# Performance work log

Hardware: AMD Instinct MI355X
Metric: run time of the kernel (lower is better)

Reference implementation:

```python
import jax, jax.numpy as jnp
import numpy as np

N_TOTAL = 200000
DIM = 256
N_GRAPHS = 8192
N_ITERS = 6


def setup_inputs() -> dict:
    key = jax.random.key(0)
    k1, k2, k3, k4, k5, k6 = jax.random.split(key, 6)
    x = jax.random.normal(k1, (N_TOTAL, DIM), dtype=jnp.float32)
    batch = jnp.sort(jax.random.randint(k2, (N_TOTAL,), 0, N_GRAPHS)).astype(jnp.int32)
    bound = 1.0 / np.sqrt(DIM)
    W_ih = jax.random.uniform(k3, (4 * DIM, DIM), jnp.float32, -bound, bound)
    W_hh = jax.random.uniform(k4, (4 * DIM, DIM), jnp.float32, -bound, bound)
    b_ih = jax.random.uniform(k5, (4 * DIM,), jnp.float32, -bound, bound)
    b_hh = jax.random.uniform(k6, (4 * DIM,), jnp.float32, -bound, bound)
    return {"x": x, "batch": batch, "n_graphs": N_GRAPHS,
            "W_ih": W_ih, "W_hh": W_hh, "b_ih": b_ih, "b_hh": b_hh}


def _lstm_cell(inp, h, c, W_ih, W_hh, b_ih, b_hh):
    # PyTorch LSTMCell: gates ordered i, f, g, o
    gates = inp @ W_ih.T + b_ih + h @ W_hh.T + b_hh
    i, f, g, o = jnp.split(gates, 4, axis=-1)
    c_new = jax.nn.sigmoid(f) * c + jax.nn.sigmoid(i) * jnp.tanh(g)
    h_new = jax.nn.sigmoid(o) * jnp.tanh(c_new)
    return h_new, c_new


def reference(x, batch, n_graphs, W_ih, W_hh, b_ih, b_hh):
    dim = x.shape[1]
    h = jnp.zeros((n_graphs, dim), x.dtype)
    c = jnp.zeros((n_graphs, dim), x.dtype)
    readout = jnp.zeros((n_graphs, dim), x.dtype)
    for _ in range(N_ITERS):
        # attention scores per node: <x_v, q_{g(v)}>
        scores = jnp.sum(x * h[batch], axis=-1)  # (N,)
        # torch scatter_reduce_ amax with zero init includes the 0 -> max(seg_max, 0)
        seg_max = jax.ops.segment_max(scores, batch, num_segments=n_graphs,
                                      indices_are_sorted=True)
        seg_max = jnp.maximum(seg_max, 0.0)
        e = jnp.exp(scores - seg_max[batch])
        seg_sum = jax.ops.segment_sum(e, batch, num_segments=n_graphs,
                                      indices_are_sorted=True)
        w = e / (seg_sum[batch] + 1e-8)  # (N,)
        readout = jax.ops.segment_sum(x * w[:, None], batch, num_segments=n_graphs,
                                      indices_are_sorted=True)  # (G, dim)
        h, c = _lstm_cell(readout, h, c, W_ih, W_hh, b_ih, b_hh)
    return jnp.concatenate([h, readout], axis=-1)  # (G, 2*dim)
```

## Files before the change

### kernel.cpp

```cpp
#include <hip/hip_runtime.h>
#include <hip/hip_bf16.h>
#include <hip/hip_fp16.h>
#include <stdint.h>

#define DIM 256
#define NG 8192
#define KDIM 512
#define GDIM 1024
#define N_ITERS 6

#define BM 128
#define BN 128
#define BK 64

typedef __hip_bfloat16 bf16;
typedef __attribute__((ext_vector_type(8))) short bf16x8;
typedef __attribute__((ext_vector_type(4))) float f32x4;
typedef __attribute__((ext_vector_type(8))) unsigned short u16x8;
typedef __attribute__((ext_vector_type(4))) unsigned short u16x4;

__device__ __forceinline__ void async16(void* lds, const void* g) {
    __builtin_amdgcn_global_load_lds((const __attribute__((address_space(1))) void*)g,
                                     (__attribute__((address_space(3))) void*)lds, 16, 0, 0);
}
__device__ __forceinline__ float fast_sigmoid(float v) {
    return 1.0f / (1.0f + __expf(-v));
}
__device__ __forceinline__ float fast_tanh(float v) {
    float e = __expf(2.0f * v);
    return (e - 1.0f) / (e + 1.0f);
}
__device__ __forceinline__ unsigned short f2bf(float v) {
    __hip_bfloat16 t = __float2bfloat16(v);
    unsigned short u; __builtin_memcpy(&u, &t, 2); return u;
}
__device__ __forceinline__ unsigned short f2h(float v) {
    __half t = __float2half_rn(v);
    unsigned short u; __builtin_memcpy(&u, &t, 2); return u;
}
__device__ __forceinline__ float h2f(unsigned short u) {
    __half t; __builtin_memcpy(&t, &u, 2);
    return __half2float(t);
}

__global__ void k_prep(const int* __restrict__ batch, int n_nodes, int* __restrict__ offs,
                       const float* __restrict__ Wih, const float* __restrict__ Whh,
                       const float* __restrict__ bih, const float* __restrict__ bhh,
                       bf16* __restrict__ Wcat, float* __restrict__ bsum,
                       float* __restrict__ h, float* __restrict__ c, bf16* __restrict__ Acat0) {
    const int idx = blockIdx.x * blockDim.x + threadIdx.x;
    if (idx < NG * DIM) {
        h[idx] = 0.0f; c[idx] = 0.0f;
        Acat0[(size_t)(idx >> 8) * KDIM + DIM + (idx & 255)] = __float2bfloat16(0.0f);
    }
    if (idx < GDIM * KDIM) {
        const int n = idx >> 9;
        const int k = idx & (KDIM - 1);
        const int d = n >> 2, gate = n & 3;
        const int j = gate * DIM + d;
        const float v = (k < DIM) ? Wih[j * DIM + k] : Whh[j * DIM + (k - DIM)];
        Wcat[idx] = __float2bfloat16(v);
    }
    if (idx < GDIM) {
        const int d = idx >> 2, gate = idx & 3;
        const int j = gate * DIM + d;
        bsum[idx] = bih[j] + bhh[j];
    }
    if (idx < n_nodes) {
        const int b = batch[idx];
        const int bp = (idx == 0) ? -1 : batch[idx - 1];
        for (int g = bp + 1; g <= b; ++g) offs[g] = idx;
        if (idx == n_nodes - 1)
            for (int g = b + 1; g <= NG; ++g) offs[g] = n_nodes;
    }
}

template <bool FIRST, bool LAST>
__global__ __launch_bounds__(256) void k_att(const float* __restrict__ xf,
                                             unsigned short* __restrict__ xb,
                                             const float* __restrict__ h,
                                             const int* __restrict__ offs,
                                             float* __restrict__ rout,
                                             bf16* __restrict__ AcatOut) {
    const int wave = threadIdx.x >> 6;
    const int g = (blockIdx.x << 2) + wave;
    const int lane = threadIdx.x & 63;
    const int half = lane >> 5, hl = lane & 31;

    float hreg[8];
    {
        const float4 a = *(const float4*)&h[(size_t)g * DIM + hl * 8];
        const float4 b = *(const float4*)&h[(size_t)g * DIM + hl * 8 + 4];
        hreg[0] = a.x; hreg[1] = a.y; hreg[2] = a.z; hreg[3] = a.w;
        hreg[4] = b.x; hreg[5] = b.y; hreg[6] = b.z; hreg[7] = b.w;
    }

    const int start = offs[g], end = offs[g + 1];
    float racc[8] = {0, 0, 0, 0, 0, 0, 0, 0};
    float m = 0.0f;
    float s = 0.0f;

    for (int r0 = start; r0 < end; r0 += 2) {
        const int r = r0 + half;
        const bool valid = (r < end);
        float xv[8];
        float dt = 0.0f;
        if (valid) {
            if (FIRST) {
                const float4 a = *(const float4*)&xf[(size_t)r * DIM + hl * 8];
                const float4 b = *(const float4*)&xf[(size_t)r * DIM + hl * 8 + 4];
                xv[0] = a.x; xv[1] = a.y; xv[2] = a.z; xv[3] = a.w;
                xv[4] = b.x; xv[5] = b.y; xv[6] = b.z; xv[7] = b.w;
                u16x8 pk;
                #pragma unroll
                for (int j = 0; j < 8; ++j) pk[j] = f2h(xv[j]);
                *(u16x8*)&xb[(size_t)r * DIM + hl * 8] = pk;
            } else {
                const u16x8 pk = *(const u16x8*)&xb[(size_t)r * DIM + hl * 8];
                #pragma unroll
                for (int j = 0; j < 8; ++j) xv[j] = h2f(pk[j]);
            }
            #pragma unroll
            for (int j = 0; j < 8; ++j) dt = fmaf(xv[j], hreg[j], dt);
        }
        #pragma unroll
        for (int off = 16; off > 0; off >>= 1) dt += __shfl_xor(dt, off);
        if (valid) {
            const float mn = fmaxf(m, dt);
            const float al = __expf(m - mn);
            const float e  = __expf(dt - mn);
            s = s * al + e;
            #pragma unroll
            for (int j = 0; j < 8; ++j) racc[j] = fmaf(racc[j], al, e * xv[j]);
            m = mn;
        }
    }

    const float mo = __shfl_xor(m, 32);
    const float M  = fmaxf(m, mo);
    const float al = __expf(m - M);
    s *= al;
    #pragma unroll
    for (int j = 0; j < 8; ++j) racc[j] *= al;
    s += __shfl_xor(s, 32);
    #pragma unroll
    for (int j = 0; j < 8; ++j) racc[j] += __shfl_xor(racc[j], 32);
    const float inv = 1.0f / (s + 1e-8f);
    float o[8];
    #pragma unroll
    for (int j = 0; j < 8; ++j) o[j] = racc[j] * inv;

    if (half == 0) {
        u16x8 pk;
        #pragma unroll
        for (int j = 0; j < 8; ++j) pk[j] = f2bf(o[j]);
        *(u16x8*)&AcatOut[(size_t)g * KDIM + hl * 8] = pk;
    } else if (LAST) {
        *(float4*)&rout[(size_t)g * KDIM + hl * 8]     = make_float4(o[0], o[1], o[2], o[3]);
        *(float4*)&rout[(size_t)g * KDIM + hl * 8 + 4] = make_float4(o[4], o[5], o[6], o[7]);
    }
}

template <bool LAST>
__global__ __launch_bounds__(256) void k_gemm_cell(const bf16* __restrict__ A,
                                                   const bf16* __restrict__ W,
                                                   const float* __restrict__ bsum,
                                                   float* __restrict__ cst,
                                                   float* __restrict__ hst,
                                                   bf16* __restrict__ AcatN,
                                                   float* __restrict__ hout) {
    __shared__ union {
        struct { bf16 As[BM * BK]; bf16 Bs[BN * BK]; } st;
        float ep[32][132];
    } sm;

    const int tid = threadIdx.x;
    const int wave = tid >> 6, lane = tid & 63;
    const int m0 = blockIdx.x * BM;
    const int n0 = blockIdx.y * BN;
    const int wr = wave >> 1, wc = wave & 1;

    f32x4 acc[4][4] = {};
    const int chunk = lane & 7;

    for (int k0 = 0; k0 < KDIM; k0 += BK) {
        #pragma unroll
        for (int i = 0; i < 4; ++i) {
            const int grp = wave * 32 + i * 8;
            async16(&sm.st.As[grp * BK],
                    A + (size_t)(m0 + grp + (lane >> 3)) * KDIM + k0 + chunk * 8);
        }
        #pragma unroll
        for (int i = 0; i < 4; ++i) {
            const int grp = wave * 32 + i * 8;
            async16(&sm.st.Bs[grp * BK],
                    W + (size_t)(n0 + grp + (lane >> 3)) * KDIM + k0 + chunk * 8);
        }
        asm volatile("s_waitcnt vmcnt(0)" ::: "memory");
        __syncthreads();

        #pragma unroll
        for (int ks = 0; ks < BK; ks += 32) {
            bf16x8 a[4], b[4];
            #pragma unroll
            for (int mi = 0; mi < 4; ++mi)
                a[mi] = *(const bf16x8*)&sm.st.As[(wr * 64 + mi * 16 + (lane & 15)) * BK + ks + (lane >> 4) * 8];
            #pragma unroll
            for (int ni = 0; ni < 4; ++ni)
                b[ni] = *(const bf16x8*)&sm.st.Bs[(wc * 64 + ni * 16 + (lane & 15)) * BK + ks + (lane >> 4) * 8];
            #pragma unroll
            for (int mi = 0; mi < 4; ++mi)
                #pragma unroll
                for (int ni = 0; ni < 4; ++ni)
                    acc[mi][ni] = __builtin_amdgcn_mfma_f32_16x16x32_bf16(a[mi], b[ni], acc[mi][ni], 0, 0, 0);
        }
        __syncthreads();
    }

    float bv[4];
    #pragma unroll
    for (int ni = 0; ni < 4; ++ni)
        bv[ni] = bsum[n0 + wc * 64 + ni * 16 + (lane & 15)];

    const int d0 = n0 >> 2;
    const int lr = tid >> 3;
    const int dd = (tid & 7) * 4;

    #pragma unroll
    for (int mi = 0; mi < 4; ++mi) {
        __syncthreads();
        #pragma unroll
        for (int ni = 0; ni < 4; ++ni) {
            const int colL = wc * 64 + ni * 16 + (lane & 15);
            #pragma unroll
            for (int r = 0; r < 4; ++r) {
                const int lrow = wr * 16 + (lane >> 4) * 4 + r;
                sm.ep[lrow][colL] = acc[mi][ni][r] + bv[ni];
            }
        }
        __syncthreads();
        const int grow = m0 + (lr >> 4) * 64 + mi * 16 + (lr & 15);
        const int d = d0 + dd;
        float co[4], cn[4], hn[4];
        *(float4*)co = *(const float4*)&cst[(size_t)grow * DIM + d];
        u16x4 hb;
        #pragma unroll
        for (int j = 0; j < 4; ++j) {
            const float4 q = *(const float4*)&sm.ep[lr][(dd + j) * 4];
            cn[j] = fast_sigmoid(q.y) * co[j] + fast_sigmoid(q.x) * fast_tanh(q.z);
            hn[j] = fast_sigmoid(q.w) * fast_tanh(cn[j]);
            hb[j] = f2bf(hn[j]);
        }
        if (LAST) {
            *(float4*)&hout[(size_t)grow * KDIM + d] = *(float4*)hn;
        } else {
            *(float4*)&cst[(size_t)grow * DIM + d] = *(float4*)cn;
            *(float4*)&hst[(size_t)grow * DIM + d] = *(float4*)hn;
            *(u16x4*)&AcatN[(size_t)grow * KDIM + DIM + d] = hb;
        }
    }
}

extern "C" void kernel_launch(void* const* d_in, const int* in_sizes, int n_in,
                              void* d_out, int out_size, void* d_ws, size_t ws_size,
                              hipStream_t stream) {
    const float* x     = (const float*)d_in[0];
    const int*   batch = (const int*)d_in[1];
    const float* Wih   = (const float*)d_in[3];
    const float* Whh   = (const float*)d_in[4];
    const float* bih   = (const float*)d_in[5];
    const float* bhh   = (const float*)d_in[6];
    const int n_nodes  = in_sizes[0] / DIM;
    float* out = (float*)d_out;

    char* ws = (char*)d_ws;
    size_t off = 0;
    auto alloc = [&](size_t bytes) -> void* {
        off = (off + 255) & ~(size_t)255;
        void* p = ws + off;
        off += bytes;
        return p;
    };
    int*   offs  = (int*)  alloc((size_t)(NG + 1) * sizeof(int));
    bf16*  Wcat  = (bf16*) alloc((size_t)GDIM * KDIM * sizeof(bf16));
    float* bsum  = (float*)alloc((size_t)GDIM * sizeof(float));
    bf16*  Acat0 = (bf16*) alloc((size_t)NG * KDIM * sizeof(bf16));
    bf16*  Acat1 = (bf16*) alloc((size_t)NG * KDIM * sizeof(bf16));
    float* h     = (float*)alloc((size_t)NG * DIM * sizeof(float));
    float* c     = (float*)alloc((size_t)NG * DIM * sizeof(float));
    unsigned short* xb = (unsigned short*)alloc((size_t)n_nodes * DIM * sizeof(unsigned short));
    (void)ws_size; (void)n_in; (void)out_size;

    k_prep<<<NG * DIM / 256, 256, 0, stream>>>(batch, n_nodes, offs, Wih, Whh, bih, bhh,
                                               Wcat, bsum, h, c, Acat0);

    for (int it = 0; it < N_ITERS; ++it) {
        bf16* Ain  = (it & 1) ? Acat1 : Acat0;
        bf16* Aout = (it & 1) ? Acat0 : Acat1;
        if (it == 0)
            k_att<true, false><<<NG / 4, 256, 0, stream>>>(x, xb, h, offs, nullptr, Ain);
        else if (it < N_ITERS - 1)
            k_att<false, false><<<NG / 4, 256, 0, stream>>>(x, xb, h, offs, nullptr, Ain);
        else
            k_att<false, true><<<NG / 4, 256, 0, stream>>>(x, xb, h, offs, out + DIM, Ain);

        if (it < N_ITERS - 1)
            k_gemm_cell<false><<<dim3(NG / BM, GDIM / BN), 256, 0, stream>>>(
                Ain, Wcat, bsum, c, h, Aout, nullptr);
        else
            k_gemm_cell<true><<<dim3(NG / BM, GDIM / BN), 256, 0, stream>>>(
                Ain, Wcat, bsum, c, nullptr, nullptr, out);
    }
}
```

Measured before the change: 832.5 us.

## Fuse all phases into one persistent cooperative kernel with grid syncs

Replaces the 13 separate launches (prep, attention and GEMM+cell per iteration) with a single cooperative kernel of 512 blocks that separates phases with grid.sync. Each wave now handles four graphs in the attention phase, and the next row's x load is software-prefetched while the current one is processed. The aim is to remove launch gaps and tail effects between phases. The cost is fewer resident waves for the memory-bound attention phase, grid-wide barrier overhead, and a launch-bounds occupancy constraint of two blocks per CU that may limit GEMM registers. A fallback path with normal launches runs if the cooperative launch fails.

```diff
diff --git a/kernel.cpp b/kernel.cpp
--- a/kernel.cpp
+++ b/kernel.cpp
@@ -1,4 +1,5 @@
 #include <hip/hip_runtime.h>
+#include <hip/hip_cooperative_groups.h>
 #include <hip/hip_bf16.h>
 #include <hip/hip_fp16.h>
 #include <stdint.h>
@@ -12,6 +13,9 @@
 #define BM 128
 #define BN 128
 #define BK 64
+#define GRID_BLOCKS 512
+
+namespace cg = cooperative_groups;
 
 typedef __hip_bfloat16 bf16;
 typedef __attribute__((ext_vector_type(8))) short bf16x8;
@@ -19,6 +23,24 @@
 typedef __attribute__((ext_vector_type(8))) unsigned short u16x8;
 typedef __attribute__((ext_vector_type(4))) unsigned short u16x4;
 
+struct Pm {
+    const float* xf; const int* batch;
+    const float* Wih; const float* Whh; const float* bih; const float* bhh;
+    int n_nodes;
+    float* out;
+    int* offs; bf16* Wcat; float* bsum;
+    bf16* Acat0; bf16* Acat1;
+    float* h; float* c;
+    unsigned short* xb;
+};
+
+struct SMU {
+    union {
+        struct { bf16 As[BM * BK]; bf16 Bs[BN * BK]; } st;
+        float ep[32][132];
+    };
+};
+
 __device__ __forceinline__ void async16(void* lds, const void* g) {
     __builtin_amdgcn_global_load_lds((const __attribute__((address_space(1))) void*)g,
                                      (__attribute__((address_space(3))) void*)lds, 16, 0, 0);
@@ -43,142 +65,137 @@
     return __half2float(t);
 }
 
-__global__ void k_prep(const int* __restrict__ batch, int n_nodes, int* __restrict__ offs,
-                       const float* __restrict__ Wih, const float* __restrict__ Whh,
-                       const float* __restrict__ bih, const float* __restrict__ bhh,
-                       bf16* __restrict__ Wcat, float* __restrict__ bsum,
-                       float* __restrict__ h, float* __restrict__ c, bf16* __restrict__ Acat0) {
-    const int idx = blockIdx.x * blockDim.x + threadIdx.x;
-    if (idx < NG * DIM) {
-        h[idx] = 0.0f; c[idx] = 0.0f;
-        Acat0[(size_t)(idx >> 8) * KDIM + DIM + (idx & 255)] = __float2bfloat16(0.0f);
-    }
-    if (idx < GDIM * KDIM) {
-        const int n = idx >> 9;
-        const int k = idx & (KDIM - 1);
+__device__ __forceinline__ void do_prep(const Pm& p) {
+    const int tid = blockIdx.x * 256 + threadIdx.x;
+    const int NT = gridDim.x * 256;
+    for (int i = tid; i < NG * DIM; i += NT) {
+        p.h[i] = 0.0f; p.c[i] = 0.0f;
+        p.Acat0[(size_t)(i >> 8) * KDIM + DIM + (i & 255)] = __float2bfloat16(0.0f);
+    }
+    for (int i = tid; i < GDIM * KDIM; i += NT) {
+        const int n = i >> 9, k = i & (KDIM - 1);
         const int d = n >> 2, gate = n & 3;
         const int j = gate * DIM + d;
-        const float v = (k < DIM) ? Wih[j * DIM + k] : Whh[j * DIM + (k - DIM)];
-        Wcat[idx] = __float2bfloat16(v);
-    }
-    if (idx < GDIM) {
-        const int d = idx >> 2, gate = idx & 3;
-        const int j = gate * DIM + d;
-        bsum[idx] = bih[j] + bhh[j];
-    }
-    if (idx < n_nodes) {
-        const int b = batch[idx];
-        const int bp = (idx == 0) ? -1 : batch[idx - 1];
-        for (int g = bp + 1; g <= b; ++g) offs[g] = idx;
-        if (idx == n_nodes - 1)
-            for (int g = b + 1; g <= NG; ++g) offs[g] = n_nodes;
+        const float v = (k < DIM) ? p.Wih[j * DIM + k] : p.Whh[j * DIM + k - DIM];
+        p.Wcat[i] = __float2bfloat16(v);
+    }
+    if (tid < GDIM) {
+        const int d = tid >> 2, gate = tid & 3;
+        p.bsum[tid] = p.bih[gate * DIM + d] + p.bhh[gate * DIM + d];
+    }
+    for (int i = tid; i < p.n_nodes; i += NT) {
+        const int b = p.batch[i];
+        const int bp = (i == 0) ? -1 : p.batch[i - 1];
+        for (int g2 = bp + 1; g2 <= b; ++g2) p.offs[g2] = i;
+        if (i == p.n_nodes - 1)
+            for (int g2 = b + 1; g2 <= NG; ++g2) p.offs[g2] = p.n_nodes;
+    }
+}
+
+template <bool FIRST>
+__device__ __forceinline__ void load_row(const Pm& p, int r, int hl, float xv[8]) {
+    if (FIRST) {
+        const float4 a = *(const float4*)&p.xf[(size_t)r * DIM + hl * 8];
+        const float4 b = *(const float4*)&p.xf[(size_t)r * DIM + hl * 8 + 4];
+        xv[0] = a.x; xv[1] = a.y; xv[2] = a.z; xv[3] = a.w;
+        xv[4] = b.x; xv[5] = b.y; xv[6] = b.z; xv[7] = b.w;
+        u16x8 pk;
+        #pragma unroll
+        for (int j = 0; j < 8; ++j) pk[j] = f2h(xv[j]);
+        *(u16x8*)&p.xb[(size_t)r * DIM + hl * 8] = pk;
+    } else {
+        const u16x8 pk = *(const u16x8*)&p.xb[(size_t)r * DIM + hl * 8];
+        #pragma unroll
+        for (int j = 0; j < 8; ++j) xv[j] = h2f(pk[j]);
     }
 }
 
 template <bool FIRST, bool LAST>
-__global__ __launch_bounds__(256) void k_att(const float* __restrict__ xf,
-                                             unsigned short* __restrict__ xb,
-                                             const float* __restrict__ h,
-                                             const int* __restrict__ offs,
-                                             float* __restrict__ rout,
-                                             bf16* __restrict__ AcatOut) {
-    const int wave = threadIdx.x >> 6;
-    const int g = (blockIdx.x << 2) + wave;
-    const int lane = threadIdx.x & 63;
+__device__ __forceinline__ void att_phase(const Pm& p, bf16* AcatOut) {
+    const int wave = threadIdx.x >> 6, lane = threadIdx.x & 63;
     const int half = lane >> 5, hl = lane & 31;
-
-    float hreg[8];
-    {
-        const float4 a = *(const float4*)&h[(size_t)g * DIM + hl * 8];
-        const float4 b = *(const float4*)&h[(size_t)g * DIM + hl * 8 + 4];
-        hreg[0] = a.x; hreg[1] = a.y; hreg[2] = a.z; hreg[3] = a.w;
-        hreg[4] = b.x; hreg[5] = b.y; hreg[6] = b.z; hreg[7] = b.w;
-    }
-
-    const int start = offs[g], end = offs[g + 1];
-    float racc[8] = {0, 0, 0, 0, 0, 0, 0, 0};
-    float m = 0.0f;
-    float s = 0.0f;
-
-    for (int r0 = start; r0 < end; r0 += 2) {
-        const int r = r0 + half;
-        const bool valid = (r < end);
+    const int wg = blockIdx.x * 4 + wave;
+
+    for (int gi = 0; gi < 4; ++gi) {
+        const int g = wg * 4 + gi;
+        float hreg[8];
+        {
+            const float4 a = *(const float4*)&p.h[(size_t)g * DIM + hl * 8];
+            const float4 b = *(const float4*)&p.h[(size_t)g * DIM + hl * 8 + 4];
+            hreg[0] = a.x; hreg[1] = a.y; hreg[2] = a.z; hreg[3] = a.w;
+            hreg[4] = b.x; hreg[5] = b.y; hreg[6] = b.z; hreg[7] = b.w;
+        }
+        const int start = p.offs[g], end = p.offs[g + 1];
+        float racc[8] = {0, 0, 0, 0, 0, 0, 0, 0};
+        float m = 0.0f;
+        float s = 0.0f;
+
         float xv[8];
-        float dt = 0.0f;
-        if (valid) {
-            if (FIRST) {
-                const float4 a = *(const float4*)&xf[(size_t)r * DIM + hl * 8];
-                const float4 b = *(const float4*)&xf[(size_t)r * DIM + hl * 8 + 4];
-                xv[0] = a.x; xv[1] = a.y; xv[2] = a.z; xv[3] = a.w;
-                xv[4] = b.x; xv[5] = b.y; xv[6] = b.z; xv[7] = b.w;
-                u16x8 pk;
+        {
+            const int r = start + half;
+            if (r < end) load_row<FIRST>(p, r, hl, xv);
+        }
+        for (int r0 = start; r0 < end; r0 += 2) {
+            const int r = r0 + half;
+            const bool valid = (r < end);
+            float cur[8];
+            #pragma unroll
+            for (int j = 0; j < 8; ++j) cur[j] = xv[j];
+            const int rn = r0 + 2 + half;
+            if (rn < end) load_row<FIRST>(p, rn, hl, xv);
+            float dt = 0.0f;
+            if (valid) {
                 #pragma unroll
-                for (int j = 0; j < 8; ++j) pk[j] = f2h(xv[j]);
-                *(u16x8*)&xb[(size_t)r * DIM + hl * 8] = pk;
-            } else {
-                const u16x8 pk = *(const u16x8*)&xb[(size_t)r * DIM + hl * 8];
+                for (int j = 0; j < 8; ++j) dt = fmaf(cur[j], hreg[j], dt);
+            }
+            #pragma unroll
+            for (int off = 16; off > 0; off >>= 1) dt += __shfl_xor(dt, off);
+            if (valid) {
+                const float mn = fmaxf(m, dt);
+                const float al = __expf(m - mn);
+                const float e  = __expf(dt - mn);
+                s = s * al + e;
                 #pragma unroll
-                for (int j = 0; j < 8; ++j) xv[j] = h2f(pk[j]);
+                for (int j = 0; j < 8; ++j) racc[j] = fmaf(racc[j], al, e * cur[j]);
+                m = mn;
             }
-            #pragma unroll
-            for (int j = 0; j < 8; ++j) dt = fmaf(xv[j], hreg[j], dt);
-        }
-        #pragma unroll
-        for (int off = 16; off > 0; off >>= 1) dt += __shfl_xor(dt, off);
-        if (valid) {
-            const float mn = fmaxf(m, dt);
-            const float al = __expf(m - mn);
-            const float e  = __expf(dt - mn);
-            s = s * al + e;
-            #pragma unroll
-            for (int j = 0; j < 8; ++j) racc[j] = fmaf(racc[j], al, e * xv[j]);
-            m = mn;
-        }
-    }
-
-    const float mo = __shfl_xor(m, 32);
-    const float M  = fmaxf(m, mo);
-    const float al = __expf(m - M);
-    s *= al;
-    #pragma unroll
-    for (int j = 0; j < 8; ++j) racc[j] *= al;
-    s += __shfl_xor(s, 32);
-    #pragma unroll
-    for (int j = 0; j < 8; ++j) racc[j] += __shfl_xor(racc[j], 32);
-    const float inv = 1.0f / (s + 1e-8f);
-    float o[8];
-    #pragma unroll
-    for (int j = 0; j < 8; ++j) o[j] = racc[j] * inv;
-
-    if (half == 0) {
-        u16x8 pk;
-        #pragma unroll
-        for (int j = 0; j < 8; ++j) pk[j] = f2bf(o[j]);
-        *(u16x8*)&AcatOut[(size_t)g * KDIM + hl * 8] = pk;
-    } else if (LAST) {
-        *(float4*)&rout[(size_t)g * KDIM + hl * 8]     = make_float4(o[0], o[1], o[2], o[3]);
-        *(float4*)&rout[(size_t)g * KDIM + hl * 8 + 4] = make_float4(o[4], o[5], o[6], o[7]);
+        }
+
+        const float mo = __shfl_xor(m, 32);
+        const float M  = fmaxf(m, mo);
+        const float al = __expf(m - M);
+        s *= al;
+        #pragma unroll
+        for (int j = 0; j < 8; ++j) racc[j] *= al;
+        s += __shfl_xor(s, 32);
+        #pragma unroll
+        for (int j = 0; j < 8; ++j) racc[j] += __shfl_xor(racc[j], 32);
+        const float inv = 1.0f / (s + 1e-8f);
+        float o[8];
+        #pragma unroll
+        for (int j = 0; j < 8; ++j) o[j] = racc[j] * inv;
+
+        if (half == 0) {
+            u16x8 pk;
+            #pragma unroll
+            for (int j = 0; j < 8; ++j) pk[j] = f2bf(o[j]);
+            *(u16x8*)&AcatOut[(size_t)g * KDIM + hl * 8] = pk;
+        } else if (LAST) {
+            float* rout = p.out + DIM;
+            *(float4*)&rout[(size_t)g * KDIM + hl * 8]     = make_float4(o[0], o[1], o[2], o[3]);
+            *(float4*)&rout[(size_t)g * KDIM + hl * 8 + 4] = make_float4(o[4], o[5], o[6], o[7]);
+        }
     }
 }
 
 template <bool LAST>
-__global__ __launch_bounds__(256) void k_gemm_cell(const bf16* __restrict__ A,
-                                                   const bf16* __restrict__ W,
-                                                   const float* __restrict__ bsum,
-                                                   float* __restrict__ cst,
-                                                   float* __restrict__ hst,
-                                                   bf16* __restrict__ AcatN,
-                                                   float* __restrict__ hout) {
-    __shared__ union {
-        struct { bf16 As[BM * BK]; bf16 Bs[BN * BK]; } st;
-        float ep[32][132];
-    } sm;
-
+__device__ __forceinline__ void gemm_phase(const Pm& p, SMU& sm, const bf16* A, bf16* AcatN) {
     const int tid = threadIdx.x;
     const int wave = tid >> 6, lane = tid & 63;
-    const int m0 = blockIdx.x * BM;
-    const int n0 = blockIdx.y * BN;
+    const int m0 = (blockIdx.x >> 3) * BM;
+    const int n0 = (blockIdx.x & 7) * BN;
     const int wr = wave >> 1, wc = wave & 1;
+    const bf16* W = p.Wcat;
 
     f32x4 acc[4][4] = {};
     const int chunk = lane & 7;
@@ -220,7 +237,7 @@
     float bv[4];
     #pragma unroll
     for (int ni = 0; ni < 4; ++ni)
-        bv[ni] = bsum[n0 + wc * 64 + ni * 16 + (lane & 15)];
+        bv[ni] = p.bsum[n0 + wc * 64 + ni * 16 + (lane & 15)];
 
     const int d0 = n0 >> 2;
     const int lr = tid >> 3;
@@ -242,7 +259,7 @@
         const int grow = m0 + (lr >> 4) * 64 + mi * 16 + (lr & 15);
         const int d = d0 + dd;
         float co[4], cn[4], hn[4];
-        *(float4*)co = *(const float4*)&cst[(size_t)grow * DIM + d];
+        *(float4*)co = *(const float4*)&p.c[(size_t)grow * DIM + d];
         u16x4 hb;
         #pragma unroll
         for (int j = 0; j < 4; ++j) {
@@ -252,27 +269,49 @@
             hb[j] = f2bf(hn[j]);
         }
         if (LAST) {
-            *(float4*)&hout[(size_t)grow * KDIM + d] = *(float4*)hn;
+            *(float4*)&p.out[(size_t)grow * KDIM + d] = *(float4*)hn;
         } else {
-            *(float4*)&cst[(size_t)grow * DIM + d] = *(float4*)cn;
-            *(float4*)&hst[(size_t)grow * DIM + d] = *(float4*)hn;
+            *(float4*)&p.c[(size_t)grow * DIM + d] = *(float4*)cn;
+            *(float4*)&p.h[(size_t)grow * DIM + d] = *(float4*)hn;
             *(u16x4*)&AcatN[(size_t)grow * KDIM + DIM + d] = hb;
         }
     }
+}
+
+__global__ __launch_bounds__(256, 2) void k_fused(Pm p) {
+    cg::grid_group grid = cg::this_grid();
+    __shared__ SMU sm;
+
+    do_prep(p);
+    grid.sync();
+
+    for (int it = 0; it < N_ITERS; ++it) {
+        bf16* Ain  = (it & 1) ? p.Acat1 : p.Acat0;
+        bf16* Aout = (it & 1) ? p.Acat0 : p.Acat1;
+        if (it == 0)               att_phase<true,  false>(p, Ain);
+        else if (it < N_ITERS - 1) att_phase<false, false>(p, Ain);
+        else                       att_phase<false, true >(p, Ain);
+        grid.sync();
+        if (it < N_ITERS - 1) gemm_phase<false>(p, sm, Ain, Aout);
+        else                  gemm_phase<true >(p, sm, Ain, nullptr);
+        grid.sync();
+    }
+}
+
+__global__ __launch_bounds__(256, 2) void k_prep_f(Pm p) { do_prep(p); }
+template <bool FIRST, bool LAST>
+__global__ __launch_bounds__(256, 2) void k_att_f(Pm p, bf16* Aout) {
+    att_phase<FIRST, LAST>(p, Aout);
+}
+template <bool LAST>
+__global__ __launch_bounds__(256, 2) void k_gemm_f(Pm p, const bf16* Ain, bf16* Aout) {
+    __shared__ SMU sm;
+    gemm_phase<LAST>(p, sm, Ain, Aout);
 }
 
 extern "C" void kernel_launch(void* const* d_in, const int* in_sizes, int n_in,
                               void* d_out, int out_size, void* d_ws, size_t ws_size,
                               hipStream_t stream) {
-    const float* x     = (const float*)d_in[0];
-    const int*   batch = (const int*)d_in[1];
-    const float* Wih   = (const float*)d_in[3];
-    const float* Whh   = (const float*)d_in[4];
-    const float* bih   = (const float*)d_in[5];
-    const float* bhh   = (const float*)d_in[6];
-    const int n_nodes  = in_sizes[0] / DIM;
-    float* out = (float*)d_out;
-
     char* ws = (char*)d_ws;
     size_t off = 0;
     auto alloc = [&](size_t bytes) -> void* {
@@ -281,34 +320,44 @@
         off += bytes;
         return p;
     };
-    int*   offs  = (int*)  alloc((size_t)(NG + 1) * sizeof(int));
-    bf16*  Wcat  = (bf16*) alloc((size_t)GDIM * KDIM * sizeof(bf16));
-    float* bsum  = (float*)alloc((size_t)GDIM * sizeof(float));
-    bf16*  Acat0 = (bf16*) alloc((size_t)NG * KDIM * sizeof(bf16));
-    bf16*  Acat1 = (bf16*) alloc((size_t)NG * KDIM * sizeof(bf16));
-    float* h     = (float*)alloc((size_t)NG * DIM * sizeof(float));
-    float* c     = (float*)alloc((size_t)NG * DIM * sizeof(float));
-    unsigned short* xb = (unsigned short*)alloc((size_t)n_nodes * DIM * sizeof(unsigned short));
+
+    Pm p;
+    p.xf    = (const float*)d_in[0];
+    p.batch = (const int*)d_in[1];
+    p.Wih   = (const float*)d_in[3];
+    p.Whh   = (const float*)d_in[4];
+    p.bih   = (const float*)d_in[5];
+    p.bhh   = (const float*)d_in[6];
+    p.n_nodes = in_sizes[0] / DIM;
+    p.out   = (float*)d_out;
+    p.offs  = (int*)  alloc((size_t)(NG + 1) * sizeof(int));
+    p.Wcat  = (bf16*) alloc((size_t)GDIM * KDIM * sizeof(bf16));
+    p.bsum  = (float*)alloc((size_t)GDIM * sizeof(float));
+    p.Acat0 = (bf16*) alloc((size_t)NG * KDIM * sizeof(bf16));
+    p.Acat1 = (bf16*) alloc((size_t)NG * KDIM * sizeof(bf16));
+    p.h     = (float*)alloc((size_t)NG * DIM * sizeof(float));
+    p.c     = (float*)alloc((size_t)NG * DIM * sizeof(float));
+    p.xb    = (unsigned short*)alloc((size_t)p.n_nodes * DIM * sizeof(unsigned short));
     (void)ws_size; (void)n_in; (void)out_size;
 
-    k_prep<<<NG * DIM / 256, 256, 0, stream>>>(batch, n_nodes, offs, Wih, Whh, bih, bhh,
-                                               Wcat, bsum, h, c, Acat0);
-
-    for (int it = 0; it < N_ITERS; ++it) {
-        bf16* Ain  = (it & 1) ? Acat1 : Acat0;
-        bf16* Aout = (it & 1) ? Acat0 : Acat1;
-        if (it == 0)
-            k_att<true, false><<<NG / 4, 256, 0, stream>>>(x, xb, h, offs, nullptr, Ain);
-        else if (it < N_ITERS - 1)
-            k_att<false, false><<<NG / 4, 256, 0, stream>>>(x, xb, h, offs, nullptr, Ain);
-        else
-            k_att<false, true><<<NG / 4, 256, 0, stream>>>(x, xb, h, offs, out + DIM, Ain);
-
-        if (it < N_ITERS - 1)
-            k_gemm_cell<false><<<dim3(NG / BM, GDIM / BN), 256, 0, stream>>>(
-                Ain, Wcat, bsum, c, h, Aout, nullptr);
-        else
-            k_gemm_cell<true><<<dim3(NG / BM, GDIM / BN), 256, 0, stream>>>(
-                Ain, Wcat, bsum, c, nullptr, nullptr, out);
-    }
-}
+    void* args[] = {(void*)&p};
+    hipError_t err = hipLaunchCooperativeKernel((void*)k_fused, dim3(GRID_BLOCKS), dim3(256),
+                                                args, 0, stream);
+    if (err != hipSuccess) {
+        k_prep_f<<<GRID_BLOCKS, 256, 0, stream>>>(p);
+        for (int it = 0; it < N_ITERS; ++it) {
+            bf16* Ain  = (it & 1) ? p.Acat1 : p.Acat0;
+            bf16* Aout = (it & 1) ? p.Acat0 : p.Acat1;
+            if (it == 0)
+                k_att_f<true,  false><<<GRID_BLOCKS, 256, 0, stream>>>(p, Ain);
+            else if (it < N_ITERS - 1)
+                k_att_f<false, false><<<GRID_BLOCKS, 256, 0, stream>>>(p, Ain);
+            else
+                k_att_f<false, true ><<<GRID_BLOCKS, 256, 0, stream>>>(p, Ain);
+            if (it < N_ITERS - 1)
+                k_gemm_f<false><<<GRID_BLOCKS, 256, 0, stream>>>(p, Ain, Aout);
+            else
+                k_gemm_f<true ><<<GRID_BLOCKS, 256, 0, stream>>>(p, Ain, nullptr);
+        }
+    }
+}
```

After: 1.643 ms. +97.4%, slower.
